# Kernel optimization log

Measured on AMD Instinct MI355X. Metric: run time of the kernel, lower is better.

The kernel has to match this reference:

```python
import jax, jax.numpy as jnp
import numpy as np

B, T, D = 4, 256, 1024
E, DL, TOPK, H = 16, 64, 2, 4


def setup_inputs() -> dict:
    key = jax.random.key(0)
    ks = jax.random.split(key, 12)
    n = lambda k, s: (0.02 * jax.random.normal(k, s)).astype(jnp.float32)
    return dict(
        x=jax.random.normal(ks[0], (B, T, D), dtype=jnp.float32),
        w_down=n(ks[1], (E * DL, D)),
        pos_embed=n(ks[2], (1, E, DL)),
        gp_w=n(ks[3], (DL, D)), gp_b=jnp.zeros((DL,), jnp.float32),
        attn_in_w=n(ks[4], (3 * DL, DL)), attn_in_b=jnp.zeros((3 * DL,), jnp.float32),
        attn_out_w=n(ks[5], (DL, DL)), attn_out_b=jnp.zeros((DL,), jnp.float32),
        ln_w=jnp.ones((DL,), jnp.float32), ln_b=jnp.zeros((DL,), jnp.float32),
        ls_w=n(ks[6], (1, DL)), ls_b=jnp.zeros((1,), jnp.float32),
        g1_w=n(ks[7], (2 * DL, DL)), g1_b=jnp.zeros((2 * DL,), jnp.float32),
        g2_w=n(ks[8], (E, 2 * DL)), g2_b=jnp.zeros((E,), jnp.float32),
        w_up=n(ks[9], (E, DL, D)),
    )


def reference(x, w_down, pos_embed, gp_w, gp_b, attn_in_w, attn_in_b,
              attn_out_w, attn_out_b, ln_w, ln_b, ls_w, ls_b,
              g1_w, g1_b, g2_w, g2_b, w_up):
    Bq, Tq, Dm = x.shape
    N = Bq * Tq
    xf = x.reshape(N, Dm)
    # per-token per-expert low-rank features [N, E, DL]
    ef = (xf @ w_down.T).reshape(N, E, DL)
    # global context per batch element -> [B, DL]
    gctx = x.mean(axis=1) @ gp_w.T + gp_b
    gtok = jnp.repeat(gctx, Tq, axis=0)[:, None, :]  # [N, 1, DL]
    seq = jnp.concatenate([gtok, ef + pos_embed], axis=1)  # [N, E+1, DL]
    # tiny multihead self-attention over E+1 tokens, eval mode (no dropout)
    qkv = seq @ attn_in_w.T + attn_in_b
    q, k, v = jnp.split(qkv, 3, axis=-1)
    hd = DL // H
    sh = lambda t: t.reshape(N, E + 1, H, hd).transpose(0, 2, 1, 3)
    q, k, v = sh(q), sh(k), sh(v)
    scores = jnp.einsum('nhqd,nhkd->nhqk', q, k) / np.float32(np.sqrt(hd))
    attn = jax.nn.softmax(scores, axis=-1)
    ctx = jnp.einsum('nhqk,nhkd->nhqd', attn, v).transpose(0, 2, 1, 3).reshape(N, E + 1, DL)
    attn_out = ctx @ attn_out_w.T + attn_out_b
    h = attn_out + seq
    mu = h.mean(-1, keepdims=True)
    var = h.var(-1, keepdims=True)
    hn = (h - mu) / jnp.sqrt(var + 1e-5) * ln_w + ln_b
    refined = hn[:, 1:, :]  # drop global token -> [N, E, DL]
    local_logits = (refined @ ls_w.T + ls_b)[..., 0]  # [N, E]
    gb = jax.nn.gelu(gctx @ g1_w.T + g1_b, approximate=False) @ g2_w.T + g2_b  # [B, E]
    logits = local_logits + jnp.repeat(gb, Tq, axis=0)
    probs = jax.nn.softmax(logits, axis=-1)
    tw, ti = jax.lax.top_k(probs, TOPK)
    tw = tw / tw.sum(-1, keepdims=True)
    sel = jnp.take_along_axis(ef, ti[..., None], axis=1)  # [N, K, DL]
    act = jax.nn.gelu(sel, approximate=False)
    # gather per-token expert up-projections and batched vec-mat
    eo = jnp.einsum('nkd,nkdm->nkm', act, w_up[ti])  # [N, K, D]
    out = (eo * tw[..., None]).sum(axis=1).reshape(Bq, Tq, Dm)
    mean_prob = probs.mean(axis=0)
    one_hot = jnp.zeros_like(probs).at[jnp.arange(N)[:, None], ti].set(1.0)
    aux_loss = E * jnp.sum(mean_prob * one_hot.mean(axis=0))
    return out, aux_loss
```

## Files before the change

kernel.cpp:

```cpp
#include <hip/hip_runtime.h>
#include <math.h>

#define NB 4
#define TT 256
#define DMODEL 1024
#define NE 16
#define DLQ 64
#define NH 4
#define HD 16
#define SEQL 17
#define NTOK 1024

static constexpr size_t WS_EF    = 0;
static constexpr size_t WS_AH    = 1048576;
static constexpr size_t WS_AL    = 1572864;
static constexpr size_t WS_BH    = 2097152;
static constexpr size_t WS_BL    = 2621440;
static constexpr size_t WS_P1    = 3145728;
static constexpr size_t WS_ACT   = 4194304;
static constexpr size_t WS_AIWFH = 4259840;
static constexpr size_t WS_AIWFL = 4265984;
static constexpr size_t WS_AOWFH = 4272128;
static constexpr size_t WS_AOWFL = 4274176;
static constexpr size_t WS_PR    = 4308992;
static constexpr size_t WS_TI    = 4325376;
static constexpr size_t WS_GCTX  = 4326400;
static constexpr size_t WS_GB    = 4326656;
static constexpr size_t WS_XPART = 4465664;

typedef __attribute__((ext_vector_type(8))) short short8;
typedef __attribute__((ext_vector_type(4))) float f32x4;

__device__ __forceinline__ float gelu_exact(float x) {
    return 0.5f * x * (1.0f + erff(x * 0.70710678118654752f));
}

__device__ __forceinline__ unsigned short f2bf(float f) {
    unsigned int u = __float_as_uint(f);
    unsigned int r = (u + 0x7fffu + ((u >> 16) & 1u)) >> 16;
    return (unsigned short)r;
}
__device__ __forceinline__ float bf2f(unsigned short h) {
    return __uint_as_float(((unsigned int)h) << 16);
}

#define DPP_ADD(v, ctrl) { int _m = __builtin_amdgcn_update_dpp(0, __float_as_int(v), ctrl, 0xF, 0xF, true); \
                           v += __int_as_float(_m); }
__device__ __forceinline__ float rsum16(float v) {
    DPP_ADD(v, 0x128);
    DPP_ADD(v, 0x124);
    DPP_ADD(v, 0x122);
    DPP_ADD(v, 0x121);
    return v;
}
__device__ __forceinline__ float rsum64(float v) {
    v = rsum16(v);
    v += __shfl_xor(v, 16);
    v += __shfl_xor(v, 32);
    return v;
}

__global__ __launch_bounds__(256) void k_prep(const float* __restrict__ x,
                                              const float* __restrict__ wdn,
                                              const float* __restrict__ aiw,
                                              const float* __restrict__ aow,
                                              float* __restrict__ ws) {
    int bi = blockIdx.x;
    int tid = threadIdx.x;
    if (bi < 1024) {
        int which = bi >> 9;
        int t = (bi & 511) * 256 + tid;
        int row = t >> 7;
        int col0 = (t & 127) * 8;
        const float* src = which ? wdn : x;
        unsigned short* hp = (unsigned short*)(ws + (which ? WS_BH : WS_AH));
        unsigned short* lp = (unsigned short*)(ws + (which ? WS_BL : WS_AL));
        float4 v0 = *(const float4*)(src + (size_t)row * DMODEL + col0);
        float4 v1 = *(const float4*)(src + (size_t)row * DMODEL + col0 + 4);
        float vv[8] = {v0.x, v0.y, v0.z, v0.w, v1.x, v1.y, v1.z, v1.w};
        unsigned short h8[8], l8[8];
#pragma unroll
        for (int j = 0; j < 8; ++j) {
            h8[j] = f2bf(vv[j]);
            l8[j] = f2bf(vv[j] - bf2f(h8[j]));
        }
        int nb = row >> 6, kb = col0 >> 6;
        int st = (row & 63) >> 4;
        int ks = (col0 & 63) >> 5;
        int ln = (row & 15) + (((col0 >> 3) & 3) << 4);
        size_t off = (size_t)(nb * 16 + kb) * 4096 + st * 1024 + ks * 512 + ln * 8;
        *(short8*)(hp + off) = *(short8*)h8;
        *(short8*)(lp + off) = *(short8*)l8;
    } else if (bi == 1024) {
        unsigned short* fh = (unsigned short*)(ws + WS_AIWFH);
        unsigned short* fl = (unsigned short*)(ws + WS_AIWFL);
        for (int idx = tid; idx < 12 * 2 * 64; idx += 256) {
            int nt = idx >> 7, kf = (idx >> 6) & 1, l = idx & 63;
            int row = nt * 16 + (l & 15);
            int k = kf * 32 + ((l >> 4) << 3);
            const float* src = aiw + (size_t)row * DLQ + k;
            unsigned short h8[8], l8[8];
#pragma unroll
            for (int j = 0; j < 8; ++j) {
                h8[j] = f2bf(src[j]);
                l8[j] = f2bf(src[j] - bf2f(h8[j]));
            }
            size_t off = (size_t)(nt * 2 + kf) * 512 + l * 8;
            *(short8*)(fh + off) = *(short8*)h8;
            *(short8*)(fl + off) = *(short8*)l8;
        }
        unsigned short* gh = (unsigned short*)(ws + WS_AOWFH);
        unsigned short* gl = (unsigned short*)(ws + WS_AOWFL);
        for (int idx = tid; idx < 4 * 2 * 64; idx += 256) {
            int nt = idx >> 7, kf = (idx >> 6) & 1, l = idx & 63;
            int row = nt * 16 + (l & 15);
            int k = kf * 32 + ((l >> 4) << 3);
            const float* src = aow + (size_t)row * DLQ + k;
            unsigned short h8[8], l8[8];
#pragma unroll
            for (int j = 0; j < 8; ++j) {
                h8[j] = f2bf(src[j]);
                l8[j] = f2bf(src[j] - bf2f(h8[j]));
            }
            size_t off = (size_t)(nt * 2 + kf) * 512 + l * 8;
            *(short8*)(gh + off) = *(short8*)h8;
            *(short8*)(gl + off) = *(short8*)l8;
        }
    } else {
        int idx = bi - 1025;
        int b = idx >> 3, j = idx & 7;
        const float* xb = x + (size_t)(b * 256 + j * 32) * DMODEL + tid * 4;
        float4 acc = {0.f, 0.f, 0.f, 0.f};
#pragma unroll 8
        for (int r = 0; r < 32; ++r) {
            float4 v = *(const float4*)(xb + (size_t)r * DMODEL);
            acc.x += v.x; acc.y += v.y; acc.z += v.z; acc.w += v.w;
        }
        *(float4*)(ws + WS_XPART + (size_t)idx * DMODEL + tid * 4) = acc;
    }
}

__global__ __launch_bounds__(256) void k_ef_mfma(const float* __restrict__ gp_w,
                                                 const float* __restrict__ gp_b,
                                                 const float* __restrict__ g1_w,
                                                 const float* __restrict__ g1_b,
                                                 const float* __restrict__ g2_w,
                                                 const float* __restrict__ g2_b,
                                                 float* __restrict__ ws) {
    __shared__ __attribute__((aligned(16))) unsigned short smem[16384];
    int tid = threadIdx.x;
    int bi = blockIdx.x;

    if (bi == 512) {
        float* gcsh = (float*)smem;
        int wv = tid >> 6, l = tid & 63;
        float4 xa[4] = {{0.f,0.f,0.f,0.f},{0.f,0.f,0.f,0.f},
                        {0.f,0.f,0.f,0.f},{0.f,0.f,0.f,0.f}};
        const float* xp = ws + WS_XPART + (size_t)wv * 8 * DMODEL + l * 16;
#pragma unroll
        for (int j = 0; j < 8; ++j) {
#pragma unroll
            for (int q = 0; q < 4; ++q) {
                float4 v = *(const float4*)(xp + (size_t)j * DMODEL + q * 4);
                xa[q].x += v.x; xa[q].y += v.y; xa[q].z += v.z; xa[q].w += v.w;
            }
        }
        float xm[16];
#pragma unroll
        for (int q = 0; q < 4; ++q) {
            xm[q * 4 + 0] = xa[q].x * (1.0f / TT);
            xm[q * 4 + 1] = xa[q].y * (1.0f / TT);
            xm[q * 4 + 2] = xa[q].z * (1.0f / TT);
            xm[q * 4 + 3] = xa[q].w * (1.0f / TT);
        }
#pragma unroll 4
        for (int c = 0; c < DLQ; ++c) {
            const float* gw = gp_w + (size_t)c * DMODEL + l * 16;
            float s = 0.f;
#pragma unroll
            for (int q = 0; q < 4; ++q) {
                float4 wv4 = *(const float4*)(gw + q * 4);
                s += xm[q * 4 + 0] * wv4.x + xm[q * 4 + 1] * wv4.y +
                     xm[q * 4 + 2] * wv4.z + xm[q * 4 + 3] * wv4.w;
            }
            s = rsum64(s);
            if (l == c) {
                float v = s + gp_b[c];
                gcsh[wv * DLQ + c] = v;
                ws[WS_GCTX + wv * DLQ + c] = v;
            }
        }
        __syncthreads();
        const float* w0 = g1_w + (size_t)(2 * l) * DLQ;
        const float* w1 = g1_w + (size_t)(2 * l + 1) * DLQ;
        float s0 = 0.f, s1 = 0.f;
#pragma unroll 8
        for (int c = 0; c < DLQ; ++c) {
            float g = gcsh[wv * DLQ + c];
            s0 += g * w0[c];
            s1 += g * w1[c];
        }
        float h0 = gelu_exact(s0 + g1_b[2 * l]);
        float h1 = gelu_exact(s1 + g1_b[2 * l + 1]);
#pragma unroll
        for (int rq = 0; rq < 4; ++rq) {
            int o = rq * 4;
            float sr[4];
#pragma unroll
            for (int r = 0; r < 4; ++r)
                sr[r] = h0 * g2_w[(size_t)(o + r) * 128 + 2 * l] +
                        h1 * g2_w[(size_t)(o + r) * 128 + 2 * l + 1];
#pragma unroll
            for (int r = 0; r < 4; ++r) sr[r] = rsum64(sr[r]);
            if (l == 0) {
#pragma unroll
                for (int r = 0; r < 4; ++r)
                    ws[WS_GB + wv * NE + o + r] = sr[r] + g2_b[o + r];
            }
        }
        return;
    }

    int xcd = bi & 7;
    int g   = bi >> 3;
    int kz  = g >> 5;
    int rem = g & 31;
    int nb  = (xcd >> 1) * 4 + (rem >> 3);
    int mb  = (xcd & 1) * 8 + (rem & 7);

    const unsigned short* AhP = (const unsigned short*)(ws + WS_AH);
    const unsigned short* AlP = (const unsigned short*)(ws + WS_AL);
    const unsigned short* BhP = (const unsigned short*)(ws + WS_BH);
    const unsigned short* BlP = (const unsigned short*)(ws + WS_BL);
    int w = tid >> 6, l = tid & 63;
    int wn = (w >> 1) * 32, wm = (w & 1) * 32;
    int stA = wn >> 4, stB = wm >> 4;
    f32x4 acc00 = {0.f, 0.f, 0.f, 0.f}, acc01 = acc00, acc10 = acc00, acc11 = acc00;

    for (int it = 0; it < 8; ++it) {
        int kb = kz * 8 + it;
        const char* srcs[4] = {
            (const char*)(AhP + (size_t)(nb * 16 + kb) * 4096),
            (const char*)(AlP + (size_t)(nb * 16 + kb) * 4096),
            (const char*)(BhP + (size_t)(mb * 16 + kb) * 4096),
            (const char*)(BlP + (size_t)(mb * 16 + kb) * 4096)};
#pragma unroll
        for (int p = 0; p < 4; ++p) {
#pragma unroll
            for (int h = 0; h < 2; ++h) {
                __builtin_amdgcn_global_load_lds(
                    (const __attribute__((address_space(1))) void*)(srcs[p] + h * 4096 + tid * 16),
                    (__attribute__((address_space(3))) void*)((char*)smem + p * 8192 + h * 4096 + tid * 16),
                    16, 0, 0);
            }
        }
        __syncthreads();
        const unsigned short* Ah = smem;
        const unsigned short* Al = smem + 4096;
        const unsigned short* Bh = smem + 8192;
        const unsigned short* Bl = smem + 12288;
#pragma unroll
        for (int ks = 0; ks < 2; ++ks) {
            short8 ah0 = *(const short8*)(Ah + (stA + 0) * 1024 + ks * 512 + l * 8);
            short8 ah1 = *(const short8*)(Ah + (stA + 1) * 1024 + ks * 512 + l * 8);
            short8 al0 = *(const short8*)(Al + (stA + 0) * 1024 + ks * 512 + l * 8);
            short8 al1 = *(const short8*)(Al + (stA + 1) * 1024 + ks * 512 + l * 8);
            short8 bh0 = *(const short8*)(Bh + (stB + 0) * 1024 + ks * 512 + l * 8);
            short8 bh1 = *(const short8*)(Bh + (stB + 1) * 1024 + ks * 512 + l * 8);
            short8 bl0 = *(const short8*)(Bl + (stB + 0) * 1024 + ks * 512 + l * 8);
            short8 bl1 = *(const short8*)(Bl + (stB + 1) * 1024 + ks * 512 + l * 8);
            acc00 = __builtin_amdgcn_mfma_f32_16x16x32_bf16(ah0, bh0, acc00, 0, 0, 0);
            acc00 = __builtin_amdgcn_mfma_f32_16x16x32_bf16(al0, bh0, acc00, 0, 0, 0);
            acc00 = __builtin_amdgcn_mfma_f32_16x16x32_bf16(ah0, bl0, acc00, 0, 0, 0);
            acc01 = __builtin_amdgcn_mfma_f32_16x16x32_bf16(ah0, bh1, acc01, 0, 0, 0);
            acc01 = __builtin_amdgcn_mfma_f32_16x16x32_bf16(al0, bh1, acc01, 0, 0, 0);
            acc01 = __builtin_amdgcn_mfma_f32_16x16x32_bf16(ah0, bl1, acc01, 0, 0, 0);
            acc10 = __builtin_amdgcn_mfma_f32_16x16x32_bf16(ah1, bh0, acc10, 0, 0, 0);
            acc10 = __builtin_amdgcn_mfma_f32_16x16x32_bf16(al1, bh0, acc10, 0, 0, 0);
            acc10 = __builtin_amdgcn_mfma_f32_16x16x32_bf16(ah1, bl0, acc10, 0, 0, 0);
            acc11 = __builtin_amdgcn_mfma_f32_16x16x32_bf16(ah1, bh1, acc11, 0, 0, 0);
            acc11 = __builtin_amdgcn_mfma_f32_16x16x32_bf16(al1, bh1, acc11, 0, 0, 0);
            acc11 = __builtin_amdgcn_mfma_f32_16x16x32_bf16(ah1, bl1, acc11, 0, 0, 0);
        }
        __syncthreads();
    }
    int cr = (l >> 4) * 4, cc = l & 15;
    int n0 = nb * 64;
    float* P = ws + (kz == 0 ? WS_EF : WS_P1);
    int m0 = mb * 64;
#pragma unroll
    for (int r = 0; r < 4; ++r) {
        P[(size_t)(n0 + wn + cr + r) * DMODEL + (m0 + wm + cc)]           = acc00[r];
        P[(size_t)(n0 + wn + cr + r) * DMODEL + (m0 + wm + 16 + cc)]      = acc01[r];
        P[(size_t)(n0 + wn + 16 + cr + r) * DMODEL + (m0 + wm + cc)]      = acc10[r];
        P[(size_t)(n0 + wn + 16 + cr + r) * DMODEL + (m0 + wm + 16 + cc)] = acc11[r];
    }
}

__global__ __launch_bounds__(128) void k_attn2(const float* __restrict__ pos_embed,
                                               const float* __restrict__ attn_in_b,
                                               const float* __restrict__ attn_out_b,
                                               const float* __restrict__ ln_w,
                                               const float* __restrict__ ln_b,
                                               const float* __restrict__ ls_w,
                                               const float* __restrict__ ls_b,
                                               float* __restrict__ ws) {
    int n = blockIdx.x;
    int w = threadIdx.x >> 6;
    int l = threadIdx.x & 63;
    int b = n >> 8;

    __shared__ float qkv[SEQL * 200];
    __shared__ __attribute__((aligned(16))) char ubuf[8192];
    __shared__ __attribute__((aligned(16))) unsigned short ctxH[1024];
    __shared__ __attribute__((aligned(16))) unsigned short ctxL[1024];
    __shared__ float lgv_sh[NE];
    unsigned short* sH = (unsigned short*)ubuf;
    unsigned short* sL = (unsigned short*)(ubuf + 4096);
    float* ao = (float*)ubuf;

    float seqc[SEQL];
    {
        const float* efp0 = ws + WS_EF + (size_t)n * DMODEL;
        const float* efp1 = ws + WS_P1 + (size_t)n * DMODEL;
        float gcv = ws[WS_GCTX + b * DLQ + l];
#pragma unroll
        for (int i = 0; i < SEQL; ++i) {
            float s = (i == 0) ? gcv
                               : efp0[(i - 1) * DLQ + l] + efp1[(i - 1) * DLQ + l] +
                                 pos_embed[(i - 1) * DLQ + l];
            seqc[i] = s;
            int lo_r = w * 9, hi_r = w * 9 + 8;
            if (i >= lo_r && i <= hi_r && i < SEQL) {
                unsigned short hs = f2bf(s);
                unsigned short lsv = f2bf(s - bf2f(hs));
                int mt = i >> 4;
                int ls = (i & 15) + (((l >> 3) & 3) << 4);
                int kf = l >> 5;
                int j = l & 7;
                size_t off = (size_t)(mt * 2 + kf) * 512 + ls * 8 + j;
                sH[off] = hs;
                sL[off] = lsv;
            }
        }
    }
    __syncthreads();

    {
        const unsigned short* fh = (const unsigned short*)(ws + WS_AIWFH);
        const unsigned short* fl = (const unsigned short*)(ws + WS_AIWFL);
        f32x4 acc[6][2];
#pragma unroll
        for (int t = 0; t < 6; ++t)
#pragma unroll
            for (int m = 0; m < 2; ++m) acc[t][m] = (f32x4){0.f, 0.f, 0.f, 0.f};
#pragma unroll
        for (int kf = 0; kf < 2; ++kf) {
            short8 ah0 = *(const short8*)(sH + (0 * 2 + kf) * 512 + l * 8);
            short8 ah1 = *(const short8*)(sH + (1 * 2 + kf) * 512 + l * 8);
            short8 al0 = *(const short8*)(sL + (0 * 2 + kf) * 512 + l * 8);
            short8 al1 = *(const short8*)(sL + (1 * 2 + kf) * 512 + l * 8);
#pragma unroll
            for (int t = 0; t < 6; ++t) {
                int nt = w * 6 + t;
                short8 bh = *(const short8*)(fh + (size_t)(nt * 2 + kf) * 512 + l * 8);
                short8 bl = *(const short8*)(fl + (size_t)(nt * 2 + kf) * 512 + l * 8);
                acc[t][0] = __builtin_amdgcn_mfma_f32_16x16x32_bf16(ah0, bh, acc[t][0], 0, 0, 0);
                acc[t][0] = __builtin_amdgcn_mfma_f32_16x16x32_bf16(al0, bh, acc[t][0], 0, 0, 0);
                acc[t][0] = __builtin_amdgcn_mfma_f32_16x16x32_bf16(ah0, bl, acc[t][0], 0, 0, 0);
                acc[t][1] = __builtin_amdgcn_mfma_f32_16x16x32_bf16(ah1, bh, acc[t][1], 0, 0, 0);
                acc[t][1] = __builtin_amdgcn_mfma_f32_16x16x32_bf16(al1, bh, acc[t][1], 0, 0, 0);
                acc[t][1] = __builtin_amdgcn_mfma_f32_16x16x32_bf16(ah1, bl, acc[t][1], 0, 0, 0);
            }
        }
#pragma unroll
        for (int t = 0; t < 6; ++t) {
            int col = (w * 6 + t) * 16 + (l & 15);
            float bias = attn_in_b[col];
#pragma unroll
            for (int r = 0; r < 4; ++r) {
                int row = (l >> 4) * 4 + r;
                qkv[row * 200 + col] = acc[t][0][r] + bias;
            }
            if ((l >> 4) == 0) qkv[16 * 200 + col] = acc[t][1][0] + bias;
        }
    }
    __syncthreads();

    {
        int g = l >> 4;
        float kc[SEQL], vc[SEQL];
#pragma unroll
        for (int j = 0; j < SEQL; ++j) {
            kc[j] = qkv[j * 200 + 64 + g * 16 + (l & 15)];
            vc[j] = qkv[j * 200 + 128 + l];
        }
        for (int i = w * 8 + 1; i <= w * 8 + 8; ++i) {
            float qi = qkv[i * 200 + g * 16 + (l & 15)];
            float sj[SEQL];
#pragma unroll
            for (int j = 0; j < SEQL; ++j) {
                sj[j] = rsum16(qi * kc[j]) * 0.25f;
            }
            float m = sj[0];
#pragma unroll
            for (int j = 1; j < SEQL; ++j) m = fmaxf(m, sj[j]);
            float ssum = 0.f;
#pragma unroll
            for (int j = 0; j < SEQL; ++j) { sj[j] = __expf(sj[j] - m); ssum += sj[j]; }
            float inv = 1.f / ssum;
            float c = 0.f;
#pragma unroll
            for (int j = 0; j < SEQL; ++j) c += sj[j] * vc[j];
            c *= inv;
            unsigned short ch = f2bf(c);
            unsigned short cl = f2bf(c - bf2f(ch));
            int ls = ((i - 1) & 15) + (((l >> 3) & 3) << 4);
            int kf = l >> 5;
            int j2 = l & 7;
            size_t off = (size_t)kf * 512 + ls * 8 + j2;
            ctxH[off] = ch;
            ctxL[off] = cl;
        }
    }
    __syncthreads();

    {
        const unsigned short* gh = (const unsigned short*)(ws + WS_AOWFH);
        const unsigned short* gl = (const unsigned short*)(ws + WS_AOWFL);
        f32x4 acc[2];
        acc[0] = (f32x4){0.f, 0.f, 0.f, 0.f};
        acc[1] = acc[0];
#pragma unroll
        for (int kf = 0; kf < 2; ++kf) {
            short8 ah = *(const short8*)(ctxH + kf * 512 + l * 8);
            short8 al = *(const short8*)(ctxL + kf * 512 + l * 8);
#pragma unroll
            for (int t = 0; t < 2; ++t) {
                int nt = w * 2 + t;
                short8 bh = *(const short8*)(gh + (size_t)(nt * 2 + kf) * 512 + l * 8);
                short8 bl = *(const short8*)(gl + (size_t)(nt * 2 + kf) * 512 + l * 8);
                acc[t] = __builtin_amdgcn_mfma_f32_16x16x32_bf16(ah, bh, acc[t], 0, 0, 0);
                acc[t] = __builtin_amdgcn_mfma_f32_16x16x32_bf16(al, bh, acc[t], 0, 0, 0);
                acc[t] = __builtin_amdgcn_mfma_f32_16x16x32_bf16(ah, bl, acc[t], 0, 0, 0);
            }
        }
        __syncthreads();
#pragma unroll
        for (int t = 0; t < 2; ++t) {
            int col = (w * 2 + t) * 16 + (l & 15);
            float bias = attn_out_b[col];
#pragma unroll
            for (int r = 0; r < 4; ++r) {
                int row = (l >> 4) * 4 + r;
                ao[row * 72 + col] = acc[t][r] + bias;
            }
        }
    }
    __syncthreads();

    float rs[SEQL];
#pragma unroll
    for (int i = 1; i < SEQL; ++i) rs[i] = seqc[i] + ao[(i - 1) * 72 + l];

    float c1 = ln_w[l] * ls_w[l];
    float c1sum = rsum64(c1);
    float c0sum = rsum64(ln_b[l] * ls_w[l]);
    float lsb0 = ls_b[0];
#pragma unroll
    for (int ee = 0; ee < 8; ++ee) {
        int e = w * 8 + ee;
        float x = rs[e + 1];
        float s1 = rsum64(x);
        float s2 = rsum64(x * x);
        float s3 = rsum64(x * c1);
        float mu = s1 * (1.0f / DLQ);
        float var = s2 * (1.0f / DLQ) - mu * mu;
        float rstd = rsqrtf(var + 1e-5f);
        float lgv = rstd * (s3 - mu * c1sum) + c0sum + lsb0 + ws[WS_GB + b * NE + e];
        if (l == 0) lgv_sh[e] = lgv;
    }
    __syncthreads();

    if (w == 0) {
        float p[NE];
        float lgv[NE];
#pragma unroll
        for (int e = 0; e < NE; ++e) lgv[e] = lgv_sh[e];
        float m = lgv[0];
#pragma unroll
        for (int e = 1; e < NE; ++e) m = fmaxf(m, lgv[e]);
        float ssum = 0.f;
#pragma unroll
        for (int e = 0; e < NE; ++e) { p[e] = __expf(lgv[e] - m); ssum += p[e]; }
        float inv = 1.f / ssum;
#pragma unroll
        for (int e = 0; e < NE; ++e) p[e] *= inv;
        int t0 = 0; float b0 = p[0];
#pragma unroll
        for (int e = 1; e < NE; ++e) if (p[e] > b0) { b0 = p[e]; t0 = e; }
        int t1 = -1; float b1 = -1.f;
#pragma unroll
        for (int e = 0; e < NE; ++e) if (e != t0 && p[e] > b1) { b1 = p[e]; t1 = e; }

        float sw = b0 + b1;
        float tw0 = b0 / sw, tw1 = b1 / sw;
        unsigned short* actp = (unsigned short*)(ws + WS_ACT);
        float efv0 = ws[WS_EF + (size_t)n * DMODEL + t0 * DLQ + l] +
                     ws[WS_P1 + (size_t)n * DMODEL + t0 * DLQ + l];
        float efv1 = ws[WS_EF + (size_t)n * DMODEL + t1 * DLQ + l] +
                     ws[WS_P1 + (size_t)n * DMODEL + t1 * DLQ + l];
        actp[(size_t)(n * 2 + 0) * 64 + l] = f2bf(gelu_exact(efv0) * tw0);
        actp[(size_t)(n * 2 + 1) * 64 + l] = f2bf(gelu_exact(efv1) * tw1);
        if (l == 0) {
#pragma unroll
            for (int e = 0; e < NE; ++e) ws[WS_PR + (size_t)n * NE + e] = p[e];
            ((int*)(ws + WS_TI))[n] = t0 | (t1 << 8);
        }
    }
}

__global__ __launch_bounds__(256) void k_moe_gemm(const float* __restrict__ w_up,
                                                  float* __restrict__ ws,
                                                  float* __restrict__ out) {
    __shared__ int lst[2048];
    __shared__ int lcnt;
    __shared__ float wsum[4][NE];
    __shared__ int hist[NE];
    int tid = threadIdx.x;
    int wv = tid >> 6, l = tid & 63;

    if (blockIdx.x == NE) {
        if (blockIdx.y != 0) return;
        if (tid < NE) hist[tid] = 0;
        __syncthreads();
        {
            const int* tip = (const int*)(ws + WS_TI);
#pragma unroll
            for (int c = 0; c < 4; ++c) {
                int pk = tip[tid * 4 + c];
                atomicAdd(&hist[pk & 0xff], 1);
                atomicAdd(&hist[(pk >> 8) & 0xff], 1);
            }
        }
        float p[NE];
#pragma unroll
        for (int e = 0; e < NE; ++e) p[e] = 0.f;
        const float* pr = ws + WS_PR + (size_t)tid * 64;
#pragma unroll
        for (int r = 0; r < 4; ++r)
#pragma unroll
            for (int q = 0; q < 4; ++q) {
                float4 v = *(const float4*)(pr + r * 16 + q * 4);
                p[q * 4 + 0] += v.x; p[q * 4 + 1] += v.y;
                p[q * 4 + 2] += v.z; p[q * 4 + 3] += v.w;
            }
#pragma unroll
        for (int e = 0; e < NE; ++e) p[e] = rsum64(p[e]);
        if (l == 0) {
#pragma unroll
            for (int e = 0; e < NE; ++e) wsum[wv][e] = p[e];
        }
        __syncthreads();
        if (tid == 0) {
            float s = 0.f;
#pragma unroll
            for (int e = 0; e < NE; ++e) {
                float sp = wsum[0][e] + wsum[1][e] + wsum[2][e] + wsum[3][e];
                s += sp * (float)hist[e];
            }
            out[(size_t)NTOK * DMODEL] = (float)NE * s / ((float)NTOK * (float)NTOK);
        }
        return;
    }

    int e = blockIdx.x, ct = blockIdx.y;
    if (tid == 0) lcnt = 0;
    __syncthreads();
    {
        const int* tip = (const int*)(ws + WS_TI);
#pragma unroll
        for (int c = 0; c < 4; ++c) {
            int tok = wv * 256 + c * 64 + l;
            int pk = tip[tok];
            bool m1 = ((pk >> 8) & 0xff) == e;
            bool m = ((pk & 0xff) == e) || m1;
            unsigned long long mask = __ballot(m);
            int base = 0;
            if (l == 0 && mask) base = atomicAdd(&lcnt, __popcll(mask));
            base = __shfl(base, 0);
            if (m) {
                int pos = base + __popcll(mask & ((1ull << l) - 1ull));
                lst[pos] = tok * 2 + (m1 ? 1 : 0);
            }
        }
    }
    __syncthreads();
    int cnt = lcnt;
    if (cnt == 0) return;

    int col = ct * 64 + wv * 16 + (l & 15);
    int kb = (l >> 4) * 8;
    const float* wue = w_up + (size_t)e * DLQ * DMODEL + col;
    unsigned short b0v[8], b1v[8];
#pragma unroll
    for (int j = 0; j < 8; ++j) {
        b0v[j] = f2bf(wue[(size_t)(kb + j) * DMODEL]);
        b1v[j] = f2bf(wue[(size_t)(kb + 32 + j) * DMODEL]);
    }
    short8 bf0 = *(short8*)b0v;
    short8 bf1 = *(short8*)b1v;

    const unsigned short* actp = (const unsigned short*)(ws + WS_ACT);
    int cr = (l >> 4) * 4;

    for (int mt = 0; mt < cnt; mt += 16) {
        int row = mt + (l & 15);
        short8 a0 = {0, 0, 0, 0, 0, 0, 0, 0};
        short8 a1 = {0, 0, 0, 0, 0, 0, 0, 0};
        if (row < cnt) {
            int pk = lst[row];
            a0 = *(const short8*)(actp + (size_t)pk * 64 + kb);
            a1 = *(const short8*)(actp + (size_t)pk * 64 + 32 + kb);
        }
        f32x4 acc = {0.f, 0.f, 0.f, 0.f};
        acc = __builtin_amdgcn_mfma_f32_16x16x32_bf16(a0, bf0, acc, 0, 0, 0);
        acc = __builtin_amdgcn_mfma_f32_16x16x32_bf16(a1, bf1, acc, 0, 0, 0);
#pragma unroll
        for (int r = 0; r < 4; ++r) {
            int rr = mt + cr + r;
            if (rr < cnt) {
                int pk = lst[rr];
                atomicAdd(&out[(size_t)(pk >> 1) * DMODEL + col], acc[r]);
            }
        }
    }
}

extern "C" void kernel_launch(void* const* d_in, const int* in_sizes, int n_in,
                              void* d_out, int out_size, void* d_ws, size_t ws_size,
                              hipStream_t stream) {
    const float* x          = (const float*)d_in[0];
    const float* w_down     = (const float*)d_in[1];
    const float* pos_embed  = (const float*)d_in[2];
    const float* gp_w       = (const float*)d_in[3];
    const float* gp_b       = (const float*)d_in[4];
    const float* attn_in_w  = (const float*)d_in[5];
    const float* attn_in_b  = (const float*)d_in[6];
    const float* attn_out_w = (const float*)d_in[7];
    const float* attn_out_b = (const float*)d_in[8];
    const float* ln_w       = (const float*)d_in[9];
    const float* ln_b       = (const float*)d_in[10];
    const float* ls_w       = (const float*)d_in[11];
    const float* ls_b       = (const float*)d_in[12];
    const float* g1_w       = (const float*)d_in[13];
    const float* g1_b       = (const float*)d_in[14];
    const float* g2_w       = (const float*)d_in[15];
    const float* g2_b       = (const float*)d_in[16];
    const float* w_up       = (const float*)d_in[17];
    float* ws  = (float*)d_ws;
    float* out = (float*)d_out;

    hipMemsetAsync(out, 0, (size_t)out_size * sizeof(float), stream);
    k_prep<<<1057, 256, 0, stream>>>(x, w_down, attn_in_w, attn_out_w, ws);
    k_ef_mfma<<<513, 256, 0, stream>>>(gp_w, gp_b, g1_w, g1_b, g2_w, g2_b, ws);
    k_attn2<<<NTOK, 128, 0, stream>>>(pos_embed, attn_in_b, attn_out_b,
                                      ln_w, ln_b, ls_w, ls_b, ws);
    k_moe_gemm<<<dim3(NE + 1, 16), 256, 0, stream>>>(w_up, ws, out);
}
```

Baseline: 182.3 us.

## Split gctx projection over four blocks and recompute gate bias inside attention kernel

The single extra block that computed the global context and the gate-bias MLP is split into four blocks, one per batch element, with each wave handling 16 output channels. The g1/g2 gate-bias MLP moves into k_attn2, where every token block recomputes it from gctx. This shortens the serial tail block in k_ef_mfma, but it adds redundant MLP work and weight reads to each of the 1024 attention blocks.

```diff
diff --git a/kernel.cpp b/kernel.cpp
--- a/kernel.cpp
+++ b/kernel.cpp
@@ -25,7 +25,6 @@
 static constexpr size_t WS_PR    = 4308992;
 static constexpr size_t WS_TI    = 4325376;
 static constexpr size_t WS_GCTX  = 4326400;
-static constexpr size_t WS_GB    = 4326656;
 static constexpr size_t WS_XPART = 4465664;
 
 typedef __attribute__((ext_vector_type(8))) short short8;
@@ -142,81 +141,46 @@
 
 __global__ __launch_bounds__(256) void k_ef_mfma(const float* __restrict__ gp_w,
                                                  const float* __restrict__ gp_b,
-                                                 const float* __restrict__ g1_w,
-                                                 const float* __restrict__ g1_b,
-                                                 const float* __restrict__ g2_w,
-                                                 const float* __restrict__ g2_b,
                                                  float* __restrict__ ws) {
     __shared__ __attribute__((aligned(16))) unsigned short smem[16384];
     int tid = threadIdx.x;
     int bi = blockIdx.x;
 
-    if (bi == 512) {
-        float* gcsh = (float*)smem;
+    if (bi >= 512) {
+        int q = bi - 512;
         int wv = tid >> 6, l = tid & 63;
         float4 xa[4] = {{0.f,0.f,0.f,0.f},{0.f,0.f,0.f,0.f},
                         {0.f,0.f,0.f,0.f},{0.f,0.f,0.f,0.f}};
-        const float* xp = ws + WS_XPART + (size_t)wv * 8 * DMODEL + l * 16;
+        const float* xp = ws + WS_XPART + (size_t)q * 8 * DMODEL + l * 16;
 #pragma unroll
         for (int j = 0; j < 8; ++j) {
 #pragma unroll
-            for (int q = 0; q < 4; ++q) {
-                float4 v = *(const float4*)(xp + (size_t)j * DMODEL + q * 4);
-                xa[q].x += v.x; xa[q].y += v.y; xa[q].z += v.z; xa[q].w += v.w;
+            for (int qq = 0; qq < 4; ++qq) {
+                float4 v = *(const float4*)(xp + (size_t)j * DMODEL + qq * 4);
+                xa[qq].x += v.x; xa[qq].y += v.y; xa[qq].z += v.z; xa[qq].w += v.w;
             }
         }
         float xm[16];
 #pragma unroll
-        for (int q = 0; q < 4; ++q) {
-            xm[q * 4 + 0] = xa[q].x * (1.0f / TT);
-            xm[q * 4 + 1] = xa[q].y * (1.0f / TT);
-            xm[q * 4 + 2] = xa[q].z * (1.0f / TT);
-            xm[q * 4 + 3] = xa[q].w * (1.0f / TT);
+        for (int qq = 0; qq < 4; ++qq) {
+            xm[qq * 4 + 0] = xa[qq].x * (1.0f / TT);
+            xm[qq * 4 + 1] = xa[qq].y * (1.0f / TT);
+            xm[qq * 4 + 2] = xa[qq].z * (1.0f / TT);
+            xm[qq * 4 + 3] = xa[qq].w * (1.0f / TT);
         }
 #pragma unroll 4
-        for (int c = 0; c < DLQ; ++c) {
+        for (int cq = 0; cq < 16; ++cq) {
+            int c = wv * 16 + cq;
             const float* gw = gp_w + (size_t)c * DMODEL + l * 16;
             float s = 0.f;
 #pragma unroll
-            for (int q = 0; q < 4; ++q) {
-                float4 wv4 = *(const float4*)(gw + q * 4);
-                s += xm[q * 4 + 0] * wv4.x + xm[q * 4 + 1] * wv4.y +
-                     xm[q * 4 + 2] * wv4.z + xm[q * 4 + 3] * wv4.w;
+            for (int qq = 0; qq < 4; ++qq) {
+                float4 w4 = *(const float4*)(gw + qq * 4);
+                s += xm[qq * 4 + 0] * w4.x + xm[qq * 4 + 1] * w4.y +
+                     xm[qq * 4 + 2] * w4.z + xm[qq * 4 + 3] * w4.w;
             }
             s = rsum64(s);
-            if (l == c) {
-                float v = s + gp_b[c];
-                gcsh[wv * DLQ + c] = v;
-                ws[WS_GCTX + wv * DLQ + c] = v;
-            }
-        }
-        __syncthreads();
-        const float* w0 = g1_w + (size_t)(2 * l) * DLQ;
-        const float* w1 = g1_w + (size_t)(2 * l + 1) * DLQ;
-        float s0 = 0.f, s1 = 0.f;
-#pragma unroll 8
-        for (int c = 0; c < DLQ; ++c) {
-            float g = gcsh[wv * DLQ + c];
-            s0 += g * w0[c];
-            s1 += g * w1[c];
-        }
-        float h0 = gelu_exact(s0 + g1_b[2 * l]);
-        float h1 = gelu_exact(s1 + g1_b[2 * l + 1]);
-#pragma unroll
-        for (int rq = 0; rq < 4; ++rq) {
-            int o = rq * 4;
-            float sr[4];
-#pragma unroll
-            for (int r = 0; r < 4; ++r)
-                sr[r] = h0 * g2_w[(size_t)(o + r) * 128 + 2 * l] +
-                        h1 * g2_w[(size_t)(o + r) * 128 + 2 * l + 1];
-#pragma unroll
-            for (int r = 0; r < 4; ++r) sr[r] = rsum64(sr[r]);
-            if (l == 0) {
-#pragma unroll
-                for (int r = 0; r < 4; ++r)
-                    ws[WS_GB + wv * NE + o + r] = sr[r] + g2_b[o + r];
-            }
+            if (l == 0) ws[WS_GCTX + q * DLQ + c] = s + gp_b[c];
         }
         return;
     }
@@ -304,6 +268,10 @@
                                                const float* __restrict__ ln_b,
                                                const float* __restrict__ ls_w,
                                                const float* __restrict__ ls_b,
+                                               const float* __restrict__ g1_w,
+                                               const float* __restrict__ g1_b,
+                                               const float* __restrict__ g2_w,
+                                               const float* __restrict__ g2_b,
                                                float* __restrict__ ws) {
     int n = blockIdx.x;
     int w = threadIdx.x >> 6;
@@ -315,15 +283,16 @@
     __shared__ __attribute__((aligned(16))) unsigned short ctxH[1024];
     __shared__ __attribute__((aligned(16))) unsigned short ctxL[1024];
     __shared__ float lgv_sh[NE];
+    __shared__ float hsh[128];
     unsigned short* sH = (unsigned short*)ubuf;
     unsigned short* sL = (unsigned short*)(ubuf + 4096);
     float* ao = (float*)ubuf;
 
     float seqc[SEQL];
+    float gcv = ws[WS_GCTX + b * DLQ + l];
     {
         const float* efp0 = ws + WS_EF + (size_t)n * DMODEL;
         const float* efp1 = ws + WS_P1 + (size_t)n * DMODEL;
-        float gcv = ws[WS_GCTX + b * DLQ + l];
 #pragma unroll
         for (int i = 0; i < SEQL; ++i) {
             float s = (i == 0) ? gcv
@@ -459,6 +428,27 @@
     }
     __syncthreads();
 
+    {
+#pragma unroll 4
+        for (int r = 0; r < 64; ++r) {
+            int row = w * 64 + r;
+            float s = rsum64(gcv * g1_w[(size_t)row * DLQ + l]);
+            if (l == r) hsh[row] = s + g1_b[row];
+        }
+    }
+    __syncthreads();
+    float gbv[8];
+    {
+        float h0 = gelu_exact(hsh[2 * l]);
+        float h1 = gelu_exact(hsh[2 * l + 1]);
+#pragma unroll
+        for (int oo = 0; oo < 8; ++oo) {
+            int o = w * 8 + oo;
+            gbv[oo] = rsum64(h0 * g2_w[(size_t)o * 128 + 2 * l] +
+                             h1 * g2_w[(size_t)o * 128 + 2 * l + 1]) + g2_b[o];
+        }
+    }
+
     float rs[SEQL];
 #pragma unroll
     for (int i = 1; i < SEQL; ++i) rs[i] = seqc[i] + ao[(i - 1) * 72 + l];
@@ -477,7 +467,7 @@
         float mu = s1 * (1.0f / DLQ);
         float var = s2 * (1.0f / DLQ) - mu * mu;
         float rstd = rsqrtf(var + 1e-5f);
-        float lgv = rstd * (s3 - mu * c1sum) + c0sum + lsb0 + ws[WS_GB + b * NE + e];
+        float lgv = rstd * (s3 - mu * c1sum) + c0sum + lsb0 + gbv[ee];
         if (l == 0) lgv_sh[e] = lgv;
     }
     __syncthreads();
@@ -663,8 +653,9 @@
 
     hipMemsetAsync(out, 0, (size_t)out_size * sizeof(float), stream);
     k_prep<<<1057, 256, 0, stream>>>(x, w_down, attn_in_w, attn_out_w, ws);
-    k_ef_mfma<<<513, 256, 0, stream>>>(gp_w, gp_b, g1_w, g1_b, g2_w, g2_b, ws);
+    k_ef_mfma<<<516, 256, 0, stream>>>(gp_w, gp_b, ws);
     k_attn2<<<NTOK, 128, 0, stream>>>(pos_embed, attn_in_b, attn_out_b,
-                                      ln_w, ln_b, ls_w, ls_b, ws);
+                                      ln_w, ln_b, ls_w, ls_b,
+                                      g1_w, g1_b, g2_w, g2_b, ws);
     k_moe_gemm<<<dim3(NE + 1, 16), 256, 0, stream>>>(w_up, ws, out);
 }
```

Result: no change. 185.1 us (+1.5%).
